# Performance work log

Hardware: AMD Instinct MI355X
Metric: run time of the kernel (lower is better)

Reference implementation:

```python
import jax, jax.numpy as jnp
import numpy as np

KERNELS = (2, 3, 6, 7)
ALPHA = 2.0
DT = 1.0  # time=1.0, step_size=1.0 -> one RK4 (3/8 rule) step, as torchdiffeq 'rk4'


def _conv(x, w, b):
    # x: [B,C,N,L], w: [O,I,1,k] -> valid conv over time axis
    y = jax.lax.conv_general_dilated(x, w, (1, 1), 'VALID',
                                     dimension_numbers=('NCHW', 'OIHW', 'NCHW'))
    return y + b[None, :, None, None]


def _inception(x, ws, bs):
    outs = [_conv(x, w, b) for w, b in zip(ws, bs)]
    L = outs[-1].shape[-1]  # shortest output (largest kernel=7)
    return jnp.concatenate([o[..., -L:] for o in outs], axis=1)


def _norm_adj(adj):
    A = adj + jnp.eye(adj.shape[0], dtype=adj.dtype)
    dinv = A.sum(1) ** -0.5
    return dinv[:, None] * A * dinv[None, :]  # D^-1/2 (A+I) D^-1/2


def _cgp(x, A_norm, mw, mb):
    f = lambda y: 0.5 * ALPHA * (jnp.einsum('ncwl,vw->ncvl', y, A_norm) - y)
    k1 = f(x)
    y2 = x + (DT / 3.0) * k1
    k2 = f(y2)
    y3 = x + DT * (k2 - k1 / 3.0)
    k3 = f(y3)
    y4 = x + DT * (k1 - k2 + k3)
    k4 = f(y4)
    yf = x + (DT / 8.0) * (k1 + 3.0 * (k2 + k3) + k4)
    # odefunc.out collects the state at each of the 4 f-evals, plus final state
    cat = jnp.concatenate([x, y2, y3, y4, yf], axis=1)  # [B, 5C, N, L]
    return _conv(cat, mw, mb)


def setup_inputs() -> dict:
    key = jax.random.key(0)
    B, C, N, T = 8, 64, 512, 64
    cq = C // 4
    ks = jax.random.split(key, 24)
    d = {
        'x': jax.random.normal(ks[0], (B, C, N, T), dtype=jnp.float32),
        'adj': jax.random.uniform(ks[1], (N, N), dtype=jnp.float32),
    }
    i = 2
    for branch in ('i1', 'i2'):
        for j, k in enumerate(KERNELS):
            d[f'{branch}w{j}'] = 0.1 * jax.random.normal(ks[i], (cq, C, 1, k), dtype=jnp.float32); i += 1
            d[f'{branch}b{j}'] = 0.1 * jax.random.normal(ks[i], (cq,), dtype=jnp.float32); i += 1
    d['m1w'] = 0.1 * jax.random.normal(ks[i], (C, 5 * C, 1, 1), dtype=jnp.float32); i += 1
    d['m1b'] = 0.1 * jax.random.normal(ks[i], (C,), dtype=jnp.float32); i += 1
    d['m2w'] = 0.1 * jax.random.normal(ks[i], (C, 5 * C, 1, 1), dtype=jnp.float32); i += 1
    d['m2b'] = 0.1 * jax.random.normal(ks[i], (C,), dtype=jnp.float32)
    return d


def reference(x, adj,
              i1w0, i1b0, i1w1, i1b1, i1w2, i1b2, i1w3, i1b3,
              i2w0, i2b0, i2w1, i2b1, i2w2, i2b2, i2w3, i2b3,
              m1w, m1b, m2w, m2b):
    T = x.shape[-1]  # receptive_field
    filt = jnp.tanh(_inception(x, (i1w0, i1w1, i1w2, i1w3), (i1b0, i1b1, i1b2, i1b3)))
    gate = jax.nn.sigmoid(_inception(x, (i2w0, i2w1, i2w2, i2w3), (i2b0, i2b1, i2b2, i2b3)))
    h = filt * gate  # dropout is identity in eval mode
    An = _norm_adj(adj)
    AnT = _norm_adj(adj.T)
    h = _cgp(h, An, m1w, m1b) + _cgp(h, AnT, m2w, m2b)
    pad = T - h.shape[-1]
    return jnp.pad(h, ((0, 0), (0, 0), (0, 0), (pad, 0)))
```

## Files before the change

kernel.cpp:

```cpp
#include <hip/hip_runtime.h>
#include <math.h>

#define NN 512
#define BB 8
#define CC 64
#define TT 64
#define LL 58
#define CL (CC*LL)
#define BCL (BB*CC*LL)
#define SZ ((size_t)NN*BCL)

typedef _Float16 half8 __attribute__((ext_vector_type(8)));
typedef _Float16 half4 __attribute__((ext_vector_type(4)));
typedef float f32x4 __attribute__((ext_vector_type(4)));

__global__ __launch_bounds__(64) void prep_adj(const float* __restrict__ adj,
                                               float* __restrict__ dinv1,
                                               float* __restrict__ dinv2){
  int v = blockIdx.x;
  int lane = threadIdx.x;
  float rs = 0.f, cs = 0.f;
  for (int w = lane; w < NN; w += 64){
    rs += adj[v*NN + w];
    cs += adj[w*NN + v];
  }
  for (int off = 32; off > 0; off >>= 1){
    rs += __shfl_down(rs, off);
    cs += __shfl_down(cs, off);
  }
  if (lane == 0){
    dinv1[v] = 1.f / sqrtf(rs + 1.f);
    dinv2[v] = 1.f / sqrtf(cs + 1.f);
  }
}

__global__ __launch_bounds__(256) void build_norm(const float* __restrict__ adj,
                                                  const float* __restrict__ dinv1,
                                                  const float* __restrict__ dinv2,
                                                  _Float16* __restrict__ An,
                                                  _Float16* __restrict__ AnT){
  int v = blockIdx.x;
  float d1v = dinv1[v], d2v = dinv2[v];
  for (int w = threadIdx.x; w < NN; w += 256){
    float diag = (v == w) ? 1.f : 0.f;
    An[v*NN + w]  = (_Float16)(d1v * (adj[v*NN + w] + diag) * dinv1[w] - diag);
    AnT[v*NN + w] = (_Float16)(d2v * (adj[w*NN + v] + diag) * dinv2[w] - diag);
  }
}

__global__ __launch_bounds__(256) void u_prep(const float* __restrict__ W1,
                                              const float* __restrict__ W2,
                                              _Float16* __restrict__ U1,
                                              _Float16* __restrict__ U2){
  const float coef[5][5] = {
    {1.f, 1.f, 1.f, 1.f, 1.f},
    {0.f, 1.f/3.f, 2.f/3.f, 1.f, 1.f},
    {0.f, 0.f, 1.f/3.f, 1.f/3.f, 0.5f},
    {0.f, 0.f, 0.f, 1.f/3.f, 1.f/6.f},
    {0.f, 0.f, 0.f, 0.f, 1.f/24.f}};
  int idx = blockIdx.x*256 + threadIdx.x;
  int o = idx / 320, rem = idx - o*320;
  int d = rem >> 6, c = rem & 63;
  float a1 = 0.f, a2 = 0.f;
  #pragma unroll
  for (int s = 0; s < 5; ++s){
    float cf = coef[d][s];
    a1 += cf * W1[o*320 + s*64 + c];
    a2 += cf * W2[o*320 + s*64 + c];
  }
  U1[idx] = (_Float16)a1;
  U2[idx] = (_Float16)a2;
}

__global__ __launch_bounds__(448) void wfg_prep(
    const float* __restrict__ w10, const float* __restrict__ w11,
    const float* __restrict__ w12, const float* __restrict__ w13,
    const float* __restrict__ w20, const float* __restrict__ w21,
    const float* __restrict__ w22, const float* __restrict__ w23,
    const float* __restrict__ b10, const float* __restrict__ b11,
    const float* __restrict__ b12, const float* __restrict__ b13,
    const float* __restrict__ b20, const float* __restrict__ b21,
    const float* __restrict__ b22, const float* __restrict__ b23,
    _Float16* __restrict__ WfG, float* __restrict__ biasFG){
  int r = blockIdx.x;
  int t = threadIdx.x;
  int qp = t >> 6, ic = t & 63;
  int gate = r >> 6;
  int j = (r >> 4) & 3;
  int oc = r & 15;
  const int kjs[4] = {2, 3, 6, 7};
  int kj = kjs[j];
  const float* wsel = gate ? ((j==0)?w20:(j==1)?w21:(j==2)?w22:w23)
                           : ((j==0)?w10:(j==1)?w11:(j==2)?w12:w13);
  int off = 7 - kj;
  float val = (qp >= off) ? wsel[(oc*64 + ic)*kj + (qp - off)] : 0.f;
  WfG[(size_t)r*448 + t] = (_Float16)val;
  if (t == 0){
    const float* bsel = gate ? ((j==0)?b20:(j==1)?b21:(j==2)?b22:b23)
                             : ((j==0)?b10:(j==1)?b11:(j==2)?b12:b13);
    biasFG[r] = bsel[oc];
  }
}

__global__ __launch_bounds__(256) void xt_prep(const float* __restrict__ x,
                                               _Float16* __restrict__ xTg){
  __shared__ float T[64][65];
  int n = blockIdx.x;
  int b = blockIdx.y;
  int tid = threadIdx.x;
  #pragma unroll
  for (int r = 0; r < 4; ++r){
    int f = tid + r*256;
    int ic = f >> 4, t4 = f & 15;
    float4 v = *(const float4*)&x[(((size_t)(b*64 + ic))*512 + n)*64 + t4*4];
    T[ic][t4*4+0] = v.x; T[ic][t4*4+1] = v.y;
    T[ic][t4*4+2] = v.z; T[ic][t4*4+3] = v.w;
  }
  __syncthreads();
  #pragma unroll
  for (int r = 0; r < 2; ++r){
    int f = tid + r*256;
    int t = f >> 3, ch = f & 7;
    half8 hv;
    #pragma unroll
    for (int q2 = 0; q2 < 8; ++q2) hv[q2] = (_Float16)T[ch*8 + q2][t];
    *(half8*)&xTg[(((size_t)(b*64 + t))*512 + n)*64 + ch*8] = hv;
  }
}

__global__ __launch_bounds__(256, 3) void inception_mfma(
    const _Float16* __restrict__ xTg,
    const _Float16* __restrict__ WfG,
    const float* __restrict__ biasFG,
    _Float16* __restrict__ S_h){
  __shared__ _Float16 X[13*32*64];
  int nt = blockIdx.x;
  int lt = blockIdx.y;
  int b  = blockIdx.z;
  int n0 = nt*32, l0 = lt*7;
  int tid = threadIdx.x;

  int sch = tid & 7, sn = (tid >> 3) & 31;
  #pragma unroll
  for (int r = 0; r < 13; ++r){
    int t = l0 + r;
    half8 v = {};
    if (t < 64)
      v = *(const half8*)&xTg[(((size_t)(b*64 + t))*512 + n0 + sn)*64 + sch*8];
    *(half8*)&X[(size_t)(r*256 + sn*8 + (sch ^ (sn & 7)))*8] = v;
  }

  int w = tid >> 6, lane = tid & 63;
  int m = lane & 15, kg = lane >> 4;

  half8 wF[14], wG[14];
  const _Float16* wb = WfG + (size_t)(w*16 + m)*448 + kg*8;
  #pragma unroll
  for (int s = 0; s < 14; ++s){
    wF[s] = *(const half8*)(wb + s*32);
    wG[s] = *(const half8*)(wb + (size_t)64*448 + s*32);
  }
  f32x4 bF = *(const f32x4*)&biasFG[w*16 + kg*4];
  f32x4 bG = *(const f32x4*)&biasFG[64 + w*16 + kg*4];

  __syncthreads();

  for (int ll = 0; ll < 7; ++ll){
    f32x4 aF0 = {}, aF1 = {}, aG0 = {}, aG1 = {};
    #pragma unroll
    for (int s = 0; s < 14; ++s){
      int t = ll + (s >> 1);
      int c0 = (s & 1)*4 + kg;
      half8 b0 = *(half8*)&X[(size_t)(t*256 + m*8        + (c0 ^ (m & 7)))*8];
      half8 b1 = *(half8*)&X[(size_t)(t*256 + (16+m)*8   + (c0 ^ (m & 7)))*8];
      aF0 = __builtin_amdgcn_mfma_f32_16x16x32_f16(wF[s], b0, aF0, 0, 0, 0);
      aG0 = __builtin_amdgcn_mfma_f32_16x16x32_f16(wG[s], b0, aG0, 0, 0, 0);
      aF1 = __builtin_amdgcn_mfma_f32_16x16x32_f16(wF[s], b1, aF1, 0, 0, 0);
      aG1 = __builtin_amdgcn_mfma_f32_16x16x32_f16(wG[s], b1, aG1, 0, 0, 0);
    }
    int l = l0 + ll;
    if (l < LL){
      #pragma unroll
      for (int rr = 0; rr < 4; ++rr){
        int c = w*16 + kg*4 + rr;
        float F0 = aF0[rr] + bF[rr];
        float G0 = aG0[rr] + bG[rr];
        float F1 = aF1[rr] + bF[rr];
        float G1 = aG1[rr] + bG[rr];
        float h0 = (2.f*__builtin_amdgcn_rcpf(1.f + __expf(-2.f*F0)) - 1.f)
                 * __builtin_amdgcn_rcpf(1.f + __expf(-G0));
        float h1 = (2.f*__builtin_amdgcn_rcpf(1.f + __expf(-2.f*F1)) - 1.f)
                 * __builtin_amdgcn_rcpf(1.f + __expf(-G1));
        size_t base = ((size_t)(b*64 + c)*LL + l)*NN + n0;
        S_h[base + m]      = (_Float16)h0;
        S_h[base + 16 + m] = (_Float16)h1;
      }
    }
  }
}

__device__ __forceinline__ void gll16(const _Float16* g, _Float16* l){
  __builtin_amdgcn_global_load_lds(
      (const __attribute__((address_space(1))) unsigned int*)g,
      (__attribute__((address_space(3))) unsigned int*)l, 16, 0, 0);
}
#define BAR() asm volatile("s_barrier" ::: "memory")

__global__ __launch_bounds__(512, 2) void gemm_z2(
    int nx,
    const _Float16* __restrict__ A0, const _Float16* __restrict__ B0,
    _Float16* __restrict__ O0,
    const _Float16* __restrict__ A1, const _Float16* __restrict__ B1,
    _Float16* __restrict__ O1){
  __shared__ _Float16 L[65536];

  int bid = blockIdx.x;
  int q8 = gridDim.x >> 3;
  int virt = (bid & 7)*q8 + (bid >> 3);
  int y = virt & 1;
  int pair = virt >> 1;
  int x = pair % nx;
  int z = pair / nx;

  const _Float16* __restrict__ A = z ? A1 : A0;
  const _Float16* __restrict__ B = z ? B1 : B0;
  _Float16* __restrict__ O = z ? O1 : O0;

  const int m0 = x * 256;
  const int v0 = y * 256;
  const int tid = threadIdx.x;
  const int ww = tid >> 6;
  const int lane = tid & 63;
  const int lr = lane & 15;
  const int kg = lane >> 4;
  const int wv = ww >> 2;
  const int wm = ww & 3;

  const int srow = lane >> 2;
  const int gch  = (lane & 3) ^ (srow & 3);
  const _Float16* gAb = A + (size_t)(v0 + ww*32 + srow)*NN + gch*8;
  const _Float16* gBb = B + (size_t)(m0 + ww*32 + srow)*NN + gch*8;

  #define STAGE_A(tt, kk)                                                   \
    { char* l_ = (char*)L + (size_t)((tt)&1)*65536 + (size_t)(kk)*16384     \
                 + ww*2048;                                                 \
      const _Float16* g_ = gAb + (tt)*64 + (kk)*32;                         \
      gll16(g_,         (_Float16*)l_);                                     \
      gll16(g_ + 16*NN, (_Float16*)(l_ + 1024)); }
  #define STAGE_B(tt, kk)                                                   \
    { char* l_ = (char*)L + (size_t)((tt)&1)*65536 + 32768                  \
                 + (size_t)(kk)*16384 + ww*2048;                            \
      const _Float16* g_ = gBb + (tt)*64 + (kk)*32;                         \
      gll16(g_,         (_Float16*)l_);                                     \
      gll16(g_ + 16*NN, (_Float16*)(l_ + 1024)); }

  const int csw = (kg ^ (lr & 3)) * 16;
  const int aR = (wv*128 + lr)*64 + csw;
  const int bR = 32768 + (wm*64 + lr)*64 + csw;

  half8 af[4], bf[4];
  f32x4 acc[8][4] = {};

  #define LOADS_A(buf, kk, ih)                                              \
    _Pragma("unroll")                                                       \
    for (int q_ = 0; q_ < 4; ++q_)                                          \
      af[q_] = *(const half8*)((char*)L + (buf)*65536 + (kk)*16384          \
                               + aR + ((ih)*4 + q_)*1024);
  #define LOADS_B(buf, kk)                                                  \
    _Pragma("unroll")                                                       \
    for (int q_ = 0; q_ < 4; ++q_)                                          \
      bf[q_] = *(const half8*)((char*)L + (buf)*65536 + (kk)*16384          \
                               + bR + q_*1024);
  #define MFMA16(ih)                                                        \
    __builtin_amdgcn_s_setprio(1);                                          \
    _Pragma("unroll")                                                       \
    for (int i_ = 0; i_ < 4; ++i_)                                          \
      _Pragma("unroll")                                                     \
      for (int j_ = 0; j_ < 4; ++j_)                                        \
        acc[(ih)*4 + i_][j_] = __builtin_amdgcn_mfma_f32_16x16x32_f16(      \
            af[i_], bf[j_], acc[(ih)*4 + i_][j_], 0, 0, 0);                 \
    __builtin_amdgcn_s_setprio(0);

  STAGE_A(0,0) STAGE_B(0,0)
  STAGE_A(0,1) STAGE_B(0,1)
  STAGE_A(1,0) STAGE_B(1,0)
  asm volatile("s_waitcnt vmcnt(8)" ::: "memory");
  BAR();

  #pragma unroll
  for (int kt = 0; kt < 8; ++kt){
    const int buf = kt & 1;
    LOADS_A(buf, 0, 0); LOADS_B(buf, 0);
    if (kt + 1 < 8) STAGE_A(kt+1, 1)
    BAR();
    MFMA16(0);
    BAR();
    LOADS_A(buf, 0, 1);
    if (kt + 1 < 8) STAGE_B(kt+1, 1)
    BAR();
    MFMA16(1);
    if (kt < 7) { asm volatile("s_waitcnt vmcnt(8)" ::: "memory"); }
    else        { asm volatile("s_waitcnt vmcnt(0)" ::: "memory"); }
    BAR();
    LOADS_A(buf, 1, 0); LOADS_B(buf, 1);
    if (kt + 2 < 8) STAGE_A(kt+2, 0)
    BAR();
    MFMA16(0);
    BAR();
    LOADS_A(buf, 1, 1);
    if (kt + 2 < 8) STAGE_B(kt+2, 0)
    BAR();
    MFMA16(1);
    if (kt < 6)      { asm volatile("s_waitcnt vmcnt(8)" ::: "memory"); }
    else if (kt == 6){ asm volatile("s_waitcnt vmcnt(4)" ::: "memory"); }
    BAR();
  }
  #undef STAGE_A
  #undef STAGE_B
  #undef LOADS_A
  #undef LOADS_B
  #undef MFMA16

  char* Lw = (char*)L + ww*16384;
  #pragma unroll
  for (int j = 0; j < 4; ++j){
    int row = j*16 + lr;
    #pragma unroll
    for (int i = 0; i < 8; ++i){
      int c = (i*4 + kg) ^ ((lr & 7)*4);
      half4 oq;
      #pragma unroll
      for (int rr = 0; rr < 4; ++rr) oq[rr] = (_Float16)acc[i][j][rr];
      *(half4*)(Lw + row*256 + c*8) = oq;
    }
  }
  #pragma unroll
  for (int s = 0; s < 16; ++s){
    int row = s*4 + kg;
    int cc = (2*lr) ^ ((row & 7)*4);
    half8 hv = *(const half8*)(Lw + row*256 + cc*8);
    *(half8*)&O[(size_t)(m0 + wm*64 + row)*NN + v0 + wv*128 + lr*8] = hv;
  }
}

template<int PASS>
__global__ __launch_bounds__(256) void combine_mfma(
    const _Float16* __restrict__ Sh, const _Float16* __restrict__ S2,
    const _Float16* __restrict__ S3, const _Float16* __restrict__ S4,
    const _Float16* __restrict__ Sf,
    const _Float16* __restrict__ Wc,
    const float* __restrict__ bias,
    _Float16* __restrict__ tmp){
  __shared__ _Float16 Xsh[64*258];
  __shared__ _Float16 Wsh[64*72];
  __shared__ float Bsh[64];
  int v0 = blockIdx.x * 256;
  int l  = blockIdx.y;
  int b  = blockIdx.z;
  int tid = threadIdx.x;
  int w = tid >> 6, lane = tid & 63;
  int lr = lane & 15, kg = lane >> 4;

  if (tid < 64) Bsh[tid] = bias[tid];

  const _Float16* Sarr[5] = {Sh, S2, S3, S4, Sf};
  f32x4 acc[4][4] = {};

  for (int kt = 0; kt < 5; ++kt){
    const _Float16* S = Sarr[kt];
    __syncthreads();
    #pragma unroll
    for (int r = 0; r < 8; ++r){
      int f = tid + r*256;
      int c = f >> 5, ch = f & 31;
      half8 xv = *(const half8*)&S[((size_t)(b*64 + c)*58 + l)*512 + v0 + ch*8];
      *(half8*)&Xsh[c*258 + ch*8] = xv;
    }
    #pragma unroll
    for (int r = 0; r < 2; ++r){
      int f = tid + r*256;
      int o = f >> 3, ch = f & 7;
      *(half8*)&Wsh[o*72 + ch*8] = *(const half8*)&Wc[(size_t)o*320 + kt*64 + ch*8];
    }
    __syncthreads();

    #pragma unroll
    for (int ks = 0; ks < 2; ++ks){
      int k0 = ks*32;
      half8 aW[4];
      #pragma unroll
      for (int jj = 0; jj < 4; ++jj)
        aW[jj] = *(half8*)&Wsh[(jj*16 + lr)*72 + k0 + kg*8];
      #pragma unroll
      for (int vt = 0; vt < 4; ++vt){
        half8 bX;
        #pragma unroll
        for (int j = 0; j < 8; ++j)
          bX[j] = Xsh[(k0 + kg*8 + j)*258 + w*64 + vt*16 + lr];
        #pragma unroll
        for (int jj = 0; jj < 4; ++jj)
          acc[vt][jj] = __builtin_amdgcn_mfma_f32_16x16x32_f16(aW[jj], bX, acc[vt][jj], 0, 0, 0);
      }
    }
  }

  size_t rowbase = ((size_t)b*58 + l)*64;
  #pragma unroll
  for (int jj = 0; jj < 4; ++jj){
    #pragma unroll
    for (int rr = 0; rr < 4; ++rr){
      int o = jj*16 + kg*4 + rr;
      float bv = Bsh[o];
      size_t obase = (rowbase + o)*512 + v0 + w*64 + lr;
      #pragma unroll
      for (int vt = 0; vt < 4; ++vt){
        float val = acc[vt][jj][rr] + bv;
        size_t addr = obase + vt*16;
        if (PASS == 0) tmp[addr] = (_Float16)val;
        else           tmp[addr] = (_Float16)((float)tmp[addr] + val);
      }
    }
  }
}

__global__ __launch_bounds__(256) void untranspose(const _Float16* __restrict__ tmp,
                                                   float* __restrict__ out){
  __shared__ float T[58][65];
  int o = blockIdx.x;
  int b = blockIdx.y;
  int v0 = blockIdx.z * 64;
  int t = threadIdx.x;
  for (int idx = t; idx < 58*64; idx += 256){
    int lr = idx >> 6, vv = idx & 63;
    T[lr][vv] = (float)tmp[((size_t)(b*58 + lr)*64 + o)*NN + v0 + vv];
  }
  __syncthreads();
  #pragma unroll
  for (int i = 0; i < 16; ++i){
    int c = t + i*256;
    int vv = c >> 6, tt = c & 63;
    float val = (tt < 6) ? 0.f : T[tt - 6][vv];
    out[((size_t)(b*64 + o)*NN + v0 + vv)*TT + tt] = val;
  }
}

extern "C" void kernel_launch(void* const* d_in, const int* in_sizes, int n_in,
                              void* d_out, int out_size, void* d_ws, size_t ws_size,
                              hipStream_t stream){
  const float* x   = (const float*)d_in[0];
  const float* adj = (const float*)d_in[1];
  const float* w1[4] = {(const float*)d_in[2],  (const float*)d_in[4],
                        (const float*)d_in[6],  (const float*)d_in[8]};
  const float* b1[4] = {(const float*)d_in[3],  (const float*)d_in[5],
                        (const float*)d_in[7],  (const float*)d_in[9]};
  const float* w2[4] = {(const float*)d_in[10], (const float*)d_in[12],
                        (const float*)d_in[14], (const float*)d_in[16]};
  const float* b2[4] = {(const float*)d_in[11], (const float*)d_in[13],
                        (const float*)d_in[15], (const float*)d_in[17]};
  const float* m1w = (const float*)d_in[18];
  const float* m1b = (const float*)d_in[19];
  const float* m2w = (const float*)d_in[20];
  const float* m2b = (const float*)d_in[21];

  char* wsb = (char*)d_ws;
  float* dinv1 = (float*)(wsb);
  float* dinv2 = (float*)(wsb + 2048);
  _Float16* U1  = (_Float16*)(wsb + 4096);
  _Float16* U2  = (_Float16*)(wsb + 4096 + 40960);
  _Float16* Mn  = (_Float16*)(wsb + 167936);
  _Float16* MnT = (_Float16*)(wsb + 167936 + 524288);
  size_t sbytes = SZ * 2;
  char* sbase = wsb + 1216512;
  _Float16* S_h = (_Float16*)(sbase);
  _Float16* S2  = (_Float16*)(sbase + sbytes);
  _Float16* S3  = (_Float16*)(sbase + 2*sbytes);
  _Float16* S4  = (_Float16*)(sbase + 3*sbytes);
  _Float16* S5  = (_Float16*)(sbase + 4*sbytes);
  _Float16* tmp = (_Float16*)(sbase + 5*sbytes);
  _Float16* xTg = S2;
  _Float16* WfG = (_Float16*)(sbase + 6*sbytes);
  float* biasFG = (float*)(sbase + 6*sbytes + 114688);
  _Float16* M2  = (_Float16*)(sbase + 6*sbytes + 131072);
  _Float16* MT2 = (_Float16*)(sbase + 6*sbytes + 131072 + 524288);
  float* out = (float*)d_out;

  prep_adj<<<NN, 64, 0, stream>>>(adj, dinv1, dinv2);
  build_norm<<<NN, 256, 0, stream>>>(adj, dinv1, dinv2, Mn, MnT);
  gemm_z2<<<8, 512, 0, stream>>>(2, MnT, Mn, M2, Mn, MnT, MT2);
  u_prep<<<80, 256, 0, stream>>>(m1w, m2w, U1, U2);
  wfg_prep<<<128, 448, 0, stream>>>(
      w1[0],w1[1],w1[2],w1[3], w2[0],w2[1],w2[2],w2[3],
      b1[0],b1[1],b1[2],b1[3], b2[0],b2[1],b2[2],b2[3], WfG, biasFG);
  xt_prep<<<dim3(NN, BB), 256, 0, stream>>>(x, xTg);
  inception_mfma<<<dim3(16, 9, 8), 256, 0, stream>>>(xTg, WfG, biasFG, S_h);

  dim3 gc(2, LL, BB);
  for (int pass = 0; pass < 2; ++pass){
    const _Float16* Mp  = pass ? MnT : Mn;
    const _Float16* Mp2 = pass ? MT2 : M2;
    gemm_z2<<<464, 512, 0, stream>>>(116, Mp, S_h, S2, Mp2, S_h, S3);
    gemm_z2<<<464, 512, 0, stream>>>(116, Mp2, S2, S4, Mp2, S3, S5);
    if (pass == 0)
      combine_mfma<0><<<gc, 256, 0, stream>>>(S_h, S2, S3, S4, S5, U1, m1b, tmp);
    else
      combine_mfma<1><<<gc, 256, 0, stream>>>(S_h, S2, S3, S4, S5, U2, m2b, tmp);
  }
  untranspose<<<dim3(64, 8, 8), 256, 0, stream>>>(tmp, out);
}
```

Baseline: 491.7 us.

## Transpose combine tile in registers into swizzled LDS for vector B-fragment loads

The combine_mfma kernel now loads each thread's 8x8 channel/vertex block into registers and transposes it with byte-permute instructions. It stores the result to a vertex-major, XOR-swizzled LDS tile, so MFMA B fragments become single 16-byte LDS reads instead of eight scalar half reads. Weights are read straight from global into registers, which removes the W shared buffer, and a launch-bounds occupancy hint of 3 blocks is added. The trade-off is more register pressure and extra permute ALU work.

After: 471.6 us. 1.04x faster.

```diff
diff --git a/kernel.cpp b/kernel.cpp
--- a/kernel.cpp
+++ b/kernel.cpp
@@ -344,15 +344,14 @@
 }
 
 template<int PASS>
-__global__ __launch_bounds__(256) void combine_mfma(
+__global__ __launch_bounds__(256, 3) void combine_mfma(
     const _Float16* __restrict__ Sh, const _Float16* __restrict__ S2,
     const _Float16* __restrict__ S3, const _Float16* __restrict__ S4,
     const _Float16* __restrict__ Sf,
     const _Float16* __restrict__ Wc,
     const float* __restrict__ bias,
     _Float16* __restrict__ tmp){
-  __shared__ _Float16 Xsh[64*258];
-  __shared__ _Float16 Wsh[64*72];
+  __shared__ __align__(16) _Float16 Xt[256*64];
   __shared__ float Bsh[64];
   int v0 = blockIdx.x * 256;
   int l  = blockIdx.y;
@@ -363,43 +362,56 @@
 
   if (tid < 64) Bsh[tid] = bias[tid];
 
+  const int c0  = ((tid >> 3) & 7) * 8;
+  const int lv0 = (tid & 7) * 8 + w * 64;
+  const int wslot = (c0 >> 3) ^ (((lv0 >> 3) & 1) << 2);
+  const int rx = ((lr >> 3) & 1) << 2;
+
   const _Float16* Sarr[5] = {Sh, S2, S3, S4, Sf};
   f32x4 acc[4][4] = {};
 
   for (int kt = 0; kt < 5; ++kt){
     const _Float16* S = Sarr[kt];
+    unsigned xr[8][4];
+    const _Float16* gbase = &S[((size_t)(b*64 + c0)*58 + l)*512 + v0 + lv0];
+    #pragma unroll
+    for (int r = 0; r < 8; ++r)
+      *(uint4*)xr[r] = *(const uint4*)(gbase + (size_t)r*58*512);
+
     __syncthreads();
-    #pragma unroll
-    for (int r = 0; r < 8; ++r){
-      int f = tid + r*256;
-      int c = f >> 5, ch = f & 31;
-      half8 xv = *(const half8*)&S[((size_t)(b*64 + c)*58 + l)*512 + v0 + ch*8];
-      *(half8*)&Xsh[c*258 + ch*8] = xv;
+
+    #pragma unroll
+    for (int q = 0; q < 8; ++q){
+      const unsigned sel = (q & 1) ? 0x07060302u : 0x05040100u;
+      const int d2 = q >> 1;
+      uint4 y;
+      y.x = __builtin_amdgcn_perm(xr[1][d2], xr[0][d2], sel);
+      y.y = __builtin_amdgcn_perm(xr[3][d2], xr[2][d2], sel);
+      y.z = __builtin_amdgcn_perm(xr[5][d2], xr[4][d2], sel);
+      y.w = __builtin_amdgcn_perm(xr[7][d2], xr[6][d2], sel);
+      *(uint4*)((char*)Xt + (lv0 + q)*128 + wslot*16) = y;
     }
-    #pragma unroll
-    for (int r = 0; r < 2; ++r){
-      int f = tid + r*256;
-      int o = f >> 3, ch = f & 7;
-      *(half8*)&Wsh[o*72 + ch*8] = *(const half8*)&Wc[(size_t)o*320 + kt*64 + ch*8];
-    }
-    __syncthreads();
-
-    #pragma unroll
-    for (int ks = 0; ks < 2; ++ks){
-      int k0 = ks*32;
-      half8 aW[4];
+
+    half8 aW[2][4];
+    #pragma unroll
+    for (int ks = 0; ks < 2; ++ks)
       #pragma unroll
       for (int jj = 0; jj < 4; ++jj)
-        aW[jj] = *(half8*)&Wsh[(jj*16 + lr)*72 + k0 + kg*8];
+        aW[ks][jj] = *(const half8*)&Wc[(size_t)(jj*16 + lr)*320
+                                        + kt*64 + ks*32 + kg*8];
+
+    __syncthreads();
+
+    #pragma unroll
+    for (int ks = 0; ks < 2; ++ks){
       #pragma unroll
       for (int vt = 0; vt < 4; ++vt){
-        half8 bX;
-        #pragma unroll
-        for (int j = 0; j < 8; ++j)
-          bX[j] = Xsh[(k0 + kg*8 + j)*258 + w*64 + vt*16 + lr];
+        half8 bf = *(const half8*)((char*)Xt + (w*64 + vt*16 + lr)*128
+                                   + ((ks*4 + kg) ^ rx)*16);
         #pragma unroll
         for (int jj = 0; jj < 4; ++jj)
-          acc[vt][jj] = __builtin_amdgcn_mfma_f32_16x16x32_f16(aW[jj], bX, acc[vt][jj], 0, 0, 0);
+          acc[vt][jj] = __builtin_amdgcn_mfma_f32_16x16x32_f16(
+              aW[ks][jj], bf, acc[vt][jj], 0, 0, 0);
       }
     }
   }
```
